# Kernel tuning notes

Hardware: AMD Instinct MI355X
Metric: run time of the kernel (lower is better)

Reference implementation:

```python
import jax, jax.numpy as jnp
import numpy as np

B, L, S, D, H, E, UV = 4, 2048, 2048, 1024, 8, 128, 128
ROT_DIM = H * E  # RotaryEmbedding(dim=qk_size*n_heads) applied on flattened dim


def gelu(x):
    return jax.nn.gelu(x, approximate=False)  # torch nn.GELU default (erf)


def rope(x):
    # x: [B, T, ROT_DIM]; interleaved-pair rotary (lucidrains rotary_embedding_torch default)
    T = x.shape[1]
    inv_freq = 1.0 / (10000.0 ** (jnp.arange(0, ROT_DIM, 2, dtype=jnp.float32) / ROT_DIM))
    freqs = jnp.arange(T, dtype=jnp.float32)[:, None] * inv_freq  # [T, ROT_DIM/2]
    cos = jnp.repeat(jnp.cos(freqs), 2, axis=-1)  # [T, ROT_DIM]
    sin = jnp.repeat(jnp.sin(freqs), 2, axis=-1)
    xp = x.reshape(*x.shape[:-1], ROT_DIM // 2, 2)
    x_rot = jnp.stack([-xp[..., 1], xp[..., 0]], axis=-1).reshape(x.shape)
    return x * cos + x_rot * sin


def setup_inputs() -> dict:
    key = jax.random.key(0)
    ks = jax.random.split(key, 16)
    n = lambda k, sh, s=1.0: jax.random.normal(k, sh, jnp.float32) * s
    w = 0.02
    return {
        "u": n(ks[0], (B, L, D)),
        "queries": n(ks[1], (B, L, D)),
        "keys": n(ks[2], (B, S, D)),
        "values": n(ks[3], (B, S, D)),
        "Wqk": n(ks[4], (D, H * E), w), "bqk": jnp.zeros((H * E,), jnp.float32),
        "Wv": n(ks[5], (D, H * UV), w), "bv": jnp.zeros((H * UV,), jnp.float32),
        "Wu": n(ks[6], (D, H * UV), w), "bu": jnp.zeros((H * UV,), jnp.float32),
        "Wo": n(ks[7], (H * UV, D), w), "bo": jnp.zeros((D,), jnp.float32),
        "q_gamma": jnp.ones((E,), jnp.float32), "q_beta": n(ks[8], (E,), w),
        "k_gamma": jnp.ones((E,), jnp.float32), "k_beta": n(ks[9], (E,), w),
    }


def _forward(u, queries, keys, values, Wqk, bqk, Wv, bv, Wu, bu, Wo, bo,
             q_gamma, q_beta, k_gamma, k_beta):
    # use_aff=True: shared qk projection + per-branch ScaleOffset over qk_size
    qk = gelu(queries @ Wqk + bqk)                      # [B,L,H*E]
    qk4 = qk.reshape(B, L, H, E)
    q = (qk4 * q_gamma + q_beta).reshape(B, L, H * E)
    k = (qk4 * k_gamma + k_beta).reshape(B, L, H * E)
    q = rope(q).reshape(B, L, H, E)
    k = rope(k).reshape(B, S, H, E)
    v = gelu(values @ Wv + bv).reshape(B, S, H, UV)
    # Conv1d(kernel_size=1) == pointwise linear over channels
    u_p = gelu(u @ Wu + bu).reshape(B, L, H, UV)
    scale = 1.0 / jnp.sqrt(jnp.float32(E))
    scores = jnp.einsum("blhe,bshe->bhls", q, k) * scale
    attn = jax.nn.softmax(scores, axis=-1)              # [B,H,L,S]
    ctx = jnp.einsum("bhls,bshd->blhd", attn, v)        # [B,L,H,UV]
    out = (u_p * ctx).reshape(B, L, H * UV)             # gate by u
    o = out @ Wo + bo                                   # [B,L,D]
    return o, attn


def reference(u, queries, keys, values, Wqk, bqk, Wv, bv, Wu, bu, Wo, bo,
              q_gamma, q_beta, k_gamma, k_beta):
    return _forward(u, queries, keys, values, Wqk, bqk, Wv, bv, Wu, bu, Wo, bo,
                    q_gamma, q_beta, k_gamma, k_beta)
```

## Files before the change

kernel.cpp:

```cpp
#include <hip/hip_runtime.h>
#include <hip/hip_bf16.h>
#include <math.h>

#define DEVI static __device__ __forceinline__

typedef __attribute__((ext_vector_type(4))) float f32x4;
typedef __attribute__((ext_vector_type(16))) float f32x16;
typedef __attribute__((ext_vector_type(8))) short bf16x8;
typedef __attribute__((ext_vector_type(4))) short bf16x4;

constexpr int Bc = 4, Lc = 2048, Sc = 2048, Dc = 1024, Hc = 8, Ec = 128, UVc = 128;
constexpr int HEc = Hc * Ec;
constexpr int BLc = Bc * Lc;

#define QSC (1.44269504088896340f / 11.31370849898476039f)

DEVI unsigned f2bf_bits(float f) {
  unsigned u = __builtin_bit_cast(unsigned, f);
  return (u + 0x7FFFu + ((u >> 16) & 1u)) >> 16;
}
DEVI short f2bf(float f) { return (short)f2bf_bits(f); }
DEVI float bf2f(short s) {
  return __builtin_bit_cast(float, (unsigned)((unsigned short)s) << 16);
}
DEVI float gelu_f(float x) {
  float z = fabsf(x) * 0.7071067811865476f;
  float t = __builtin_amdgcn_rcpf(1.0f + 0.3275911f * z);
  float p = t * (0.254829592f +
            t * (-0.284496736f +
            t * (1.421413741f +
            t * (-1.453152027f + t * 1.061405429f))));
  float e = exp2f(-z * z * 1.4426950408889634f);
  float er = copysignf(1.0f - p * e, x);
  return 0.5f * x * (1.0f + er);
}

DEVI void gload16(const void* gsrc, void* ldst) {
  __builtin_amdgcn_global_load_lds(
      (const __attribute__((address_space(1))) unsigned*)gsrc,
      (__attribute__((address_space(3))) unsigned*)(ldst), 16, 0, 0);
}

DEVI f32x4 mfma16(bf16x8 a, bf16x8 b, f32x4 c) {
  return __builtin_amdgcn_mfma_f32_16x16x32_bf16(a, b, c, 0, 0, 0);
}
DEVI f32x16 mfma32(bf16x8 a, bf16x8 b, f32x16 c) {
  return __builtin_amdgcn_mfma_f32_32x32x16_bf16(a, b, c, 0, 0, 0);
}

__global__ void cvt3_kernel(const float* __restrict__ i0, const float* __restrict__ i1,
                            const float* __restrict__ i2, short* __restrict__ o0,
                            short* __restrict__ o1, short* __restrict__ o2) {
  const float* ins[3] = {i0, i1, i2};
  short* outs[3] = {o0, o1, o2};
  const float* in = ins[blockIdx.y];
  short* out = outs[blockIdx.y];
  size_t i = ((size_t)blockIdx.x * 256 + threadIdx.x) * 8;
  float4 f1 = *reinterpret_cast<const float4*>(in + i);
  float4 f2 = *reinterpret_cast<const float4*>(in + i + 4);
  uint4 pk;
  pk.x = f2bf_bits(f1.x) | (f2bf_bits(f1.y) << 16);
  pk.y = f2bf_bits(f1.z) | (f2bf_bits(f1.w) << 16);
  pk.z = f2bf_bits(f2.x) | (f2bf_bits(f2.y) << 16);
  pk.w = f2bf_bits(f2.z) | (f2bf_bits(f2.w) << 16);
  *reinterpret_cast<uint4*>(out + i) = pk;
}

__global__ void prep_kernel(const float* __restrict__ W0, const float* __restrict__ W1,
                            const float* __restrict__ W2, const float* __restrict__ W3,
                            short* __restrict__ T0, short* __restrict__ T1,
                            short* __restrict__ T2, short* __restrict__ T3,
                            float2* __restrict__ cs) {
  int tx = threadIdx.x, ty = threadIdx.y;
  if (blockIdx.z == 4) {
    int base = (blockIdx.y * 32 + blockIdx.x) * 256 + ty * 32 + tx;
#pragma unroll
    for (int j = 0; j < 4; j++) {
      int idx = base + j * 262144;
      int t = idx >> 9, i = idx & 511;
      float inv = expf((float)i * (-9.210340371976184f / 512.0f));
      float sv, cv;
      sincosf((float)t * inv, &sv, &cv);
      cs[idx] = make_float2(cv, sv);
    }
    return;
  }
  __shared__ float tbuf[32][33];
  const float* Ws[4] = {W0, W1, W2, W3};
  short* Ts[4] = {T0, T1, T2, T3};
  const float* W = Ws[blockIdx.z];
  short* WT = Ts[blockIdx.z];
  int n0 = blockIdx.x * 32, k0 = blockIdx.y * 32;
#pragma unroll
  for (int i = 0; i < 4; i++) {
    int r = ty + i * 8;
    tbuf[r][tx] = W[(size_t)(k0 + r) * 1024 + n0 + tx];
  }
  __syncthreads();
#pragma unroll
  for (int i = 0; i < 4; i++) {
    int r = ty + i * 8;
    WT[(size_t)(n0 + r) * 1024 + k0 + tx] = f2bf(tbuf[tx][r]);
  }
}

template <int EPI>
__global__ __launch_bounds__(256, 3) void gemm_kernel(
    const short* __restrict__ A, const short* __restrict__ BT,
    const float* __restrict__ bias, void* __restrict__ Cptr, int M, int N, int K) {
  __shared__ char smem[49152];
  const int tid = threadIdx.x;
  const int wave = tid >> 6, lane = tid & 63;
  const int lquad = lane >> 4, l15 = lane & 15;
  const int m0 = blockIdx.x * 128, n0 = blockIdx.y * 128;
  const int wr = wave >> 1, wc = wave & 1;
  f32x4 acc[4][4] = {};

  const int q0 = tid * 16, q1 = tid * 16 + 4096;
  const int r0 = q0 >> 6, o0 = (q0 & 63) ^ ((r0 & 3) << 4);
  const int r1 = q1 >> 6, o1 = (q1 & 63) ^ ((r1 & 3) << 4);
  const short* a0 = A + (size_t)(m0 + r0) * K + (o0 >> 1);
  const short* a1 = A + (size_t)(m0 + r1) * K + (o1 >> 1);
  const short* b0 = BT + (size_t)(n0 + r0) * K + (o0 >> 1);
  const short* b1 = BT + (size_t)(n0 + r1) * K + (o1 >> 1);

#define G_STAGE(buf, kt)                     \
  {                                          \
    char* As_ = smem + (buf)*8192;           \
    char* Bs_ = smem + 24576 + (buf)*8192;   \
    gload16(a0 + (kt), As_ + q0);            \
    gload16(a1 + (kt), As_ + q1);            \
    gload16(b0 + (kt), Bs_ + q0);            \
    gload16(b1 + (kt), Bs_ + q1);            \
  }

  G_STAGE(0, 0);
  G_STAGE(1, 32);
  asm volatile("s_waitcnt vmcnt(4)" ::: "memory");
  __builtin_amdgcn_s_barrier();

  const int NT = K >> 5;
  int cur = 0;
  for (int t = 0; t < NT; t++) {
    int nb = cur + 2;
    if (nb >= 3) nb -= 3;
    G_STAGE(nb, (t + 2 < NT) ? (t + 2) * 32 : 0);
    __builtin_amdgcn_sched_barrier(0);
    const char* As_ = smem + cur * 8192;
    const char* Bs_ = smem + 24576 + cur * 8192;
    const int ko = lquad * 16;
    bf16x8 a[4], b[4];
#pragma unroll
    for (int f = 0; f < 4; f++) {
      int ra = wr * 64 + f * 16 + l15;
      a[f] = *reinterpret_cast<const bf16x8*>(As_ + ra * 64 + (ko ^ ((ra & 3) << 4)));
      int rb = wc * 64 + f * 16 + l15;
      b[f] = *reinterpret_cast<const bf16x8*>(Bs_ + rb * 64 + (ko ^ ((rb & 3) << 4)));
    }
#pragma unroll
    for (int mf = 0; mf < 4; mf++)
#pragma unroll
      for (int nf = 0; nf < 4; nf++)
        acc[mf][nf] = mfma16(a[mf], b[nf], acc[mf][nf]);
    asm volatile("s_waitcnt vmcnt(4) lgkmcnt(0)" ::: "memory");
    __builtin_amdgcn_sched_barrier(0);
    __builtin_amdgcn_s_barrier();
    cur = (cur == 2) ? 0 : cur + 1;
  }
#undef G_STAGE

#pragma unroll
  for (int mf = 0; mf < 4; mf++) {
#pragma unroll
    for (int nf = 0; nf < 4; nf++) {
      const int mrow = m0 + wr * 64 + mf * 16 + 4 * lquad;
      const int ncol = n0 + wc * 64 + nf * 16 + l15;
      const float bval = bias[ncol];
      if constexpr (EPI == 3) {
        int hh = ncol >> 7, dd = ncol & 127;
        int bb = mrow >> 11, ss = mrow & 2047;
        bf16x4 gv;
#pragma unroll
        for (int r = 0; r < 4; r++) gv[r] = f2bf(gelu_f(acc[mf][nf][r] + bval));
        *reinterpret_cast<bf16x4*>((short*)Cptr + (((size_t)bb * 8 + hh) * 128 + dd) * 2048 + ss) = gv;
      } else if constexpr (EPI == 1) {
#pragma unroll
        for (int r = 0; r < 4; r++)
          ((short*)Cptr)[(size_t)(mrow + r) * N + ncol] = f2bf(gelu_f(acc[mf][nf][r] + bval));
      } else {
#pragma unroll
        for (int r = 0; r < 4; r++)
          ((float*)Cptr)[(size_t)(mrow + r) * N + ncol] = acc[mf][nf][r] + bval;
      }
    }
  }
}

__global__ void rope_apply_kernel(const short* __restrict__ qkg,
                                  const float2* __restrict__ cstab,
                                  const float* __restrict__ qg, const float* __restrict__ qb,
                                  const float* __restrict__ kg, const float* __restrict__ kb,
                                  short* __restrict__ qo, short* __restrict__ ko) {
  int tid = blockIdx.x * 256 + threadIdx.x;
  size_t base = (size_t)tid * 8;
  int bl = (int)(base >> 10);
  int rem = (int)(base & 1023);
  int e0 = rem & 127;
  int t = bl & 2047;
  int pf = rem >> 1;
  uint4 raw = *reinterpret_cast<const uint4*>(qkg + base);
  short sh[8];
  *reinterpret_cast<uint4*>(sh) = raw;
  const float* csf = (const float*)cstab + (size_t)t * 1024 + 2 * pf;
  float4 p01 = *reinterpret_cast<const float4*>(csf);
  float4 p23 = *reinterpret_cast<const float4*>(csf + 4);
  float C[4] = {p01.x, p01.z, p23.x, p23.z};
  float Sn[4] = {p01.y, p01.w, p23.y, p23.w};
  float4 qga = *reinterpret_cast<const float4*>(qg + e0);
  float4 qgb = *reinterpret_cast<const float4*>(qg + e0 + 4);
  float4 qba = *reinterpret_cast<const float4*>(qb + e0);
  float4 qbb = *reinterpret_cast<const float4*>(qb + e0 + 4);
  float4 kga = *reinterpret_cast<const float4*>(kg + e0);
  float4 kgb = *reinterpret_cast<const float4*>(kg + e0 + 4);
  float4 kba = *reinterpret_cast<const float4*>(kb + e0);
  float4 kbb = *reinterpret_cast<const float4*>(kb + e0 + 4);
  float QG[8] = {qga.x, qga.y, qga.z, qga.w, qgb.x, qgb.y, qgb.z, qgb.w};
  float QB[8] = {qba.x, qba.y, qba.z, qba.w, qbb.x, qbb.y, qbb.z, qbb.w};
  float KG[8] = {kga.x, kga.y, kga.z, kga.w, kgb.x, kgb.y, kgb.z, kgb.w};
  float KB[8] = {kba.x, kba.y, kba.z, kba.w, kbb.x, kbb.y, kbb.z, kbb.w};
  short qsh[8], ksh[8];
#pragma unroll
  for (int j = 0; j < 4; j++) {
    float x0 = bf2f(sh[2 * j]), x1 = bf2f(sh[2 * j + 1]);
    float q0 = x0 * QG[2 * j] + QB[2 * j];
    float q1 = x1 * QG[2 * j + 1] + QB[2 * j + 1];
    qsh[2 * j] = f2bf((q0 * C[j] - q1 * Sn[j]) * QSC);
    qsh[2 * j + 1] = f2bf((q1 * C[j] + q0 * Sn[j]) * QSC);
    float k0v = x0 * KG[2 * j] + KB[2 * j];
    float k1v = x1 * KG[2 * j + 1] + KB[2 * j + 1];
    ksh[2 * j] = f2bf(k0v * C[j] - k1v * Sn[j]);
    ksh[2 * j + 1] = f2bf(k1v * C[j] + k0v * Sn[j]);
  }
  *reinterpret_cast<uint4*>(qo + base) = *reinterpret_cast<uint4*>(qsh);
  *reinterpret_cast<uint4*>(ko + base) = *reinterpret_cast<uint4*>(ksh);
}

__global__ __launch_bounds__(256, 3) void passa_kernel(
    const short* __restrict__ qs, const short* __restrict__ ks,
    float* __restrict__ rcpbuf) {
  __shared__ char smem[49152];
  const int bid = blockIdx.x;
  const int xcd = bid & 7, jj = bid >> 3;
  const int bh = xcd * 4 + (jj >> 4);
  const int lblk = jj & 15;
  const int b = bh >> 3, h = bh & 7;
  const int l0 = lblk * 128;
  const int tid = threadIdx.x;
  const int wave = tid >> 6, lane = tid & 63;
  const int l31 = lane & 31, lhg = lane >> 5;

  const short* ksrc[4];
  int kq[4];
#pragma unroll
  for (int i = 0; i < 4; i++) {
    int q = i * 4096 + tid * 16;
    kq[i] = q;
    int row = q >> 8, off = (q & 255) ^ ((row & 7) << 4);
    ksrc[i] = ks + (((size_t)b * Sc + row) * Hc + h) * Ec + (off >> 1);
  }

  bf16x8 qf[8];
  {
    const char* qp = (const char*)(qs + (((size_t)b * Lc + l0 + wave * 32 + l31) * Hc + h) * Ec);
#pragma unroll
    for (int kt = 0; kt < 8; kt++)
      qf[kt] = *reinterpret_cast<const bf16x8*>(qp + kt * 32 + 16 * lhg);
  }
  __builtin_amdgcn_sched_barrier(0);

#define STAGE_A(buf, s0)                                  \
  {                                                       \
    char* Kb_ = smem + (buf)*16384;                       \
    gload16(ksrc[0] + (size_t)(s0)*1024, Kb_ + kq[0]);    \
    gload16(ksrc[1] + (size_t)(s0)*1024, Kb_ + kq[1]);    \
    gload16(ksrc[2] + (size_t)(s0)*1024, Kb_ + kq[2]);    \
    gload16(ksrc[3] + (size_t)(s0)*1024, Kb_ + kq[3]);    \
  }

  STAGE_A(0, 0);
  STAGE_A(1, 64);
  asm volatile("s_waitcnt vmcnt(4)" ::: "memory");
  __builtin_amdgcn_s_barrier();
  float ra = 0.f, rb = 0.f, rc = 0.f, rd = 0.f;
  int cur = 0;
  for (int t = 0; t < 32; t++) {
    int nb = cur + 2;
    if (nb >= 3) nb -= 3;
    STAGE_A(nb, (t + 2 < 32) ? (t + 2) * 64 : 0);
    __builtin_amdgcn_sched_barrier(0);
    const char* KB_ = smem + cur * 16384;
    f32x16 d0 = {}, d1 = {};
    __builtin_amdgcn_s_setprio(1);
#pragma unroll
    for (int kt = 0; kt < 8; kt++) {
      int row0 = l31, row1 = 32 + l31;
      bf16x8 k0 = *reinterpret_cast<const bf16x8*>(
          KB_ + row0 * 256 + ((kt * 32 + 16 * lhg) ^ ((row0 & 7) << 4)));
      bf16x8 k1 = *reinterpret_cast<const bf16x8*>(
          KB_ + row1 * 256 + ((kt * 32 + 16 * lhg) ^ ((row1 & 7) << 4)));
      d0 = mfma32(k0, qf[kt], d0);
      d1 = mfma32(k1, qf[kt], d1);
    }
    __builtin_amdgcn_s_setprio(0);
#pragma unroll
    for (int r = 0; r < 16; r += 4) {
      ra += exp2f(d0[r]) + exp2f(d1[r]);
      rb += exp2f(d0[r + 1]) + exp2f(d1[r + 1]);
      rc += exp2f(d0[r + 2]) + exp2f(d1[r + 2]);
      rd += exp2f(d0[r + 3]) + exp2f(d1[r + 3]);
    }
    asm volatile("s_waitcnt vmcnt(4) lgkmcnt(0)" ::: "memory");
    __builtin_amdgcn_sched_barrier(0);
    __builtin_amdgcn_s_barrier();
    cur = (cur == 2) ? 0 : cur + 1;
  }
#undef STAGE_A
  float rs = (ra + rb) + (rc + rd);
  rs += __shfl_xor(rs, 32);
  if (lane < 32)
    rcpbuf[(size_t)bh * Lc + l0 + wave * 32 + l31] = 1.0f / rs;
}

__global__ __launch_bounds__(256, 3) void attn_kernel(
    const short* __restrict__ qs, const short* __restrict__ ks,
    const short* __restrict__ vT, const short* __restrict__ up,
    const float* __restrict__ rcpbuf, float* __restrict__ attn_out,
    short* __restrict__ gate) {
  __shared__ char smem[49152];
  const int bid = blockIdx.x;
  const int xcd = bid & 7, jj = bid >> 3;
  const int bh = xcd * 4 + (jj >> 4);
  const int lblk = jj & 15;
  const int b = bh >> 3, h = bh & 7;
  const int l0 = lblk * 128;
  const int tid = threadIdx.x;
  const int wave = tid >> 6, lane = tid & 63;
  const int lquad = lane >> 4, l15 = lane & 15;

  const short* ksrc[2];
  int kq[2];
#pragma unroll
  for (int i = 0; i < 2; i++) {
    int q = i * 4096 + tid * 16;
    kq[i] = q;
    int row = q >> 8, off = (q & 255) ^ ((row & 7) << 4);
    ksrc[i] = ks + (((size_t)b * Sc + row) * Hc + h) * Ec + (off >> 1);
  }
  const short* vsrc[2];
  int vq[2];
#pragma unroll
  for (int i = 0; i < 2; i++) {
    int q = i * 4096 + tid * 16;
    vq[i] = q;
    int rv = q >> 6;
    int j = (q >> 4) & 3;
    int c = (j - (rv & 3)) & 3;
    vsrc[i] = vT + ((size_t)bh * UVc + rv) * Sc + (c << 3);
  }

  bf16x8 qf[2][4];
  float rcp[2];
#pragma unroll
  for (int cf = 0; cf < 2; cf++) {
    int lrow = l0 + wave * 32 + cf * 16 + l15;
    const short* qp = qs + (((size_t)b * Lc + lrow) * Hc + h) * Ec;
#pragma unroll
    for (int kt = 0; kt < 4; kt++)
      qf[cf][kt] = *reinterpret_cast<const bf16x8*>(qp + kt * 32 + lquad * 8);
    rcp[cf] = rcpbuf[(size_t)bh * Lc + lrow];
  }
  __builtin_amdgcn_sched_barrier(0);

#define STAGE_B(buf, s0)                                  \
  {                                                       \
    char* Kb_ = smem + (buf)*8192;                        \
    char* Vb_ = smem + 24576 + (buf)*8192;                \
    gload16(ksrc[0] + (size_t)(s0)*1024, Kb_ + kq[0]);    \
    gload16(ksrc[1] + (size_t)(s0)*1024, Kb_ + kq[1]);    \
    gload16(vsrc[0] + (s0), Vb_ + vq[0]);                 \
    gload16(vsrc[1] + (s0), Vb_ + vq[1]);                 \
  }

  STAGE_B(0, 0);
  STAGE_B(1, 32);
  asm volatile("s_waitcnt vmcnt(4)" ::: "memory");
  __builtin_amdgcn_s_barrier();
  f32x4 ctx[8][2] = {};
  int cur = 0;
  for (int t = 0; t < 64; t++) {
    const int s0 = t * 32;
    const char* KB_ = smem + cur * 8192;
    const char* VB_ = smem + 24576 + cur * 8192;
    f32x4 d[2][2] = {};
    __builtin_amdgcn_s_setprio(1);
#pragma unroll
    for (int kt = 0; kt < 4; kt++)
#pragma unroll
      for (int sf = 0; sf < 2; sf++) {
        int row = sf * 16 + l15;
        bf16x8 kf = *reinterpret_cast<const bf16x8*>(
            KB_ + row * 256 + ((kt * 64 + lquad * 16) ^ ((row & 7) << 4)));
        d[sf][0] = mfma16(kf, qf[0][kt], d[sf][0]);
        d[sf][1] = mfma16(kf, qf[1][kt], d[sf][1]);
      }
    __builtin_amdgcn_s_setprio(0);
#pragma unroll
    for (int sf = 0; sf < 2; sf++)
#pragma unroll
      for (int cf = 0; cf < 2; cf++)
#pragma unroll
        for (int r = 0; r < 4; r++)
          d[sf][cf][r] = exp2f(d[sf][cf][r]) * rcp[cf];
#pragma unroll
    for (int cf = 0; cf < 2; cf++) {
      int lrow = l0 + wave * 32 + cf * 16 + l15;
      float* arow = attn_out + ((size_t)bh * Lc + lrow) * Sc + s0 + lquad * 4;
      __builtin_nontemporal_store(d[0][cf], reinterpret_cast<f32x4*>(arow));
      __builtin_nontemporal_store(d[1][cf], reinterpret_cast<f32x4*>(arow + 16));
    }
    bf16x8 pb[2];
#pragma unroll
    for (int cf = 0; cf < 2; cf++)
#pragma unroll
      for (int r = 0; r < 4; r++) {
        pb[cf][r] = f2bf(d[0][cf][r]);
        pb[cf][4 + r] = f2bf(d[1][cf][r]);
      }
    __builtin_amdgcn_s_setprio(1);
#pragma unroll
    for (int df = 0; df < 8; df++) {
      int dd = df * 16 + l15;
      const char* vrow = VB_ + dd * 64;
      int half = (lquad & 1) * 8;
      int clo = ((lquad >> 1) + (dd & 3)) & 3;
      int chi = ((lquad >> 1) + 2 + (dd & 3)) & 3;
      bf16x4 lo = *reinterpret_cast<const bf16x4*>(vrow + clo * 16 + half);
      bf16x4 hi = *reinterpret_cast<const bf16x4*>(vrow + chi * 16 + half);
      bf16x8 vf = __builtin_shufflevector(lo, hi, 0, 1, 2, 3, 4, 5, 6, 7);
      ctx[df][0] = mfma16(vf, pb[0], ctx[df][0]);
      ctx[df][1] = mfma16(vf, pb[1], ctx[df][1]);
    }
    __builtin_amdgcn_s_setprio(0);
    {
      int nb = cur + 2;
      if (nb >= 3) nb -= 3;
      STAGE_B(nb, (t + 2 < 64) ? s0 + 64 : 0);
    }
    asm volatile("s_waitcnt vmcnt(8) lgkmcnt(0)" ::: "memory");
    __builtin_amdgcn_sched_barrier(0);
    __builtin_amdgcn_s_barrier();
    cur = (cur == 2) ? 0 : cur + 1;
  }
#undef STAGE_B

#pragma unroll
  for (int cf = 0; cf < 2; cf++) {
    int lrow = l0 + wave * 32 + cf * 16 + l15;
    size_t base = ((size_t)b * Lc + lrow) * HEc + h * UVc;
    const short* ub = up + base;
    short* gp = gate + base;
#pragma unroll
    for (int df = 0; df < 8; df++) {
      int doff = df * 16 + lquad * 4;
      bf16x4 uv = *reinterpret_cast<const bf16x4*>(ub + doff);
      bf16x4 gv;
#pragma unroll
      for (int r = 0; r < 4; r++)
        gv[r] = f2bf(bf2f(uv[r]) * ctx[df][cf][r]);
      *reinterpret_cast<bf16x4*>(gp + doff) = gv;
    }
  }
}

extern "C" void kernel_launch(void* const* d_in, const int* in_sizes, int n_in,
                              void* d_out, int out_size, void* d_ws, size_t ws_size,
                              hipStream_t stream) {
  const float* u_in = (const float*)d_in[0];
  const float* qry = (const float*)d_in[1];
  const float* vals = (const float*)d_in[3];
  const float* Wqk = (const float*)d_in[4];
  const float* bqk = (const float*)d_in[5];
  const float* Wv = (const float*)d_in[6];
  const float* bv = (const float*)d_in[7];
  const float* Wu = (const float*)d_in[8];
  const float* bu = (const float*)d_in[9];
  const float* Wo = (const float*)d_in[10];
  const float* bo = (const float*)d_in[11];
  const float* qg = (const float*)d_in[12];
  const float* qb = (const float*)d_in[13];
  const float* kg = (const float*)d_in[14];
  const float* kb = (const float*)d_in[15];

  char* w = (char*)d_ws;
  short* WT0 = (short*)w; w += (size_t)1024 * 1024 * 2;
  short* WT1 = (short*)w; w += (size_t)1024 * 1024 * 2;
  short* WT2 = (short*)w; w += (size_t)1024 * 1024 * 2;
  short* WT3 = (short*)w; w += (size_t)1024 * 1024 * 2;
  float2* cstab = (float2*)w; w += (size_t)2048 * 512 * 8;
  float* rcpb = (float*)w; w += (size_t)32 * 2048 * 4;
  const size_t BUF = (size_t)BLc * HEc * 2;
  short* C1 = (short*)w; w += BUF;
  short* C2 = (short*)w; w += BUF;
  short* C3 = (short*)w; w += BUF;
  short* qkg = (short*)w; w += BUF;
  short* qbf = (short*)w; w += BUF;
  short* vTb = (short*)w; w += BUF;
  short* upb = (short*)w; w += BUF;
  short* kbf = qkg;
  short* gtb = C1;

  float* o_out = (float*)d_out;
  float* attn_out = o_out + (size_t)BLc * Dc;

  dim3 tb(32, 8);
  cvt3_kernel<<<dim3(4096, 3), 256, 0, stream>>>(qry, vals, u_in, C1, C2, C3);
  prep_kernel<<<dim3(32, 32, 5), tb, 0, stream>>>(Wqk, Wv, Wu, Wo, WT0, WT1, WT2, WT3, cstab);

  gemm_kernel<1><<<dim3(64, 8), 256, 0, stream>>>(C1, WT0, bqk, qkg, BLc, HEc, Dc);
  rope_apply_kernel<<<4096, 256, 0, stream>>>(qkg, cstab, qg, qb, kg, kb, qbf, kbf);
  passa_kernel<<<512, 256, 0, stream>>>(qbf, kbf, rcpb);
  gemm_kernel<3><<<dim3(64, 8), 256, 0, stream>>>(C2, WT1, bv, vTb, BLc, HEc, Dc);
  gemm_kernel<1><<<dim3(64, 8), 256, 0, stream>>>(C3, WT2, bu, upb, BLc, HEc, Dc);
  attn_kernel<<<512, 256, 0, stream>>>(qbf, kbf, vTb, upb, rcpb, attn_out, gtb);
  gemm_kernel<0><<<dim3(64, 8), 256, 0, stream>>>(gtb, WT3, bo, o_out, BLc, Dc, HEc);
}
```

Baseline: 387.2 us.

## Fuse RoPE and scale-offset into QK GEMM epilogue; merge prep kernels

The QK projection GEMM now applies GELU, the per-branch scale/offset and rotary embedding in its epilogue. It gets each rotary partner value via a lane xor-shuffle and writes q and k bf16 directly, so the separate rope kernel and its intermediate buffer round trip go away. The input conversion, weight transpose and cos/sin table kernels are merged into one launch to cut launch overhead. In exchange, the epilogue stores become scattered 2-byte writes and the kernel reads the cos/sin table from global memory per element.

After: 378.8 us. 1.02x faster.

```diff
diff --git a/kernel.cpp b/kernel.cpp
--- a/kernel.cpp
+++ b/kernel.cpp
@@ -48,81 +48,106 @@
   return __builtin_amdgcn_mfma_f32_32x32x16_bf16(a, b, c, 0, 0, 0);
 }
 
-__global__ void cvt3_kernel(const float* __restrict__ i0, const float* __restrict__ i1,
-                            const float* __restrict__ i2, short* __restrict__ o0,
-                            short* __restrict__ o1, short* __restrict__ o2) {
-  const float* ins[3] = {i0, i1, i2};
-  short* outs[3] = {o0, o1, o2};
-  const float* in = ins[blockIdx.y];
-  short* out = outs[blockIdx.y];
-  size_t i = ((size_t)blockIdx.x * 256 + threadIdx.x) * 8;
-  float4 f1 = *reinterpret_cast<const float4*>(in + i);
-  float4 f2 = *reinterpret_cast<const float4*>(in + i + 4);
-  uint4 pk;
-  pk.x = f2bf_bits(f1.x) | (f2bf_bits(f1.y) << 16);
-  pk.y = f2bf_bits(f1.z) | (f2bf_bits(f1.w) << 16);
-  pk.z = f2bf_bits(f2.x) | (f2bf_bits(f2.y) << 16);
-  pk.w = f2bf_bits(f2.z) | (f2bf_bits(f2.w) << 16);
-  *reinterpret_cast<uint4*>(out + i) = pk;
-}
-
-__global__ void prep_kernel(const float* __restrict__ W0, const float* __restrict__ W1,
-                            const float* __restrict__ W2, const float* __restrict__ W3,
-                            short* __restrict__ T0, short* __restrict__ T1,
-                            short* __restrict__ T2, short* __restrict__ T3,
-                            float2* __restrict__ cs) {
-  int tx = threadIdx.x, ty = threadIdx.y;
-  if (blockIdx.z == 4) {
-    int base = (blockIdx.y * 32 + blockIdx.x) * 256 + ty * 32 + tx;
+__global__ void prep_all_kernel(const float* __restrict__ in_q, const float* __restrict__ in_v,
+                                const float* __restrict__ in_u, short* __restrict__ C1,
+                                short* __restrict__ C2, short* __restrict__ C3,
+                                const float* __restrict__ W0, const float* __restrict__ W1,
+                                const float* __restrict__ W2, const float* __restrict__ W3,
+                                short* __restrict__ T0, short* __restrict__ T1,
+                                short* __restrict__ T2, short* __restrict__ T3,
+                                float2* __restrict__ cs) {
+  __shared__ float tbuf[32][33];
+  const int bid = blockIdx.x;
+  const int t = threadIdx.x;
+  if (bid < 12288) {
+    int which = bid >> 12, blk = bid & 4095;
+    const float* in = (which == 0) ? in_q : (which == 1) ? in_v : in_u;
+    short* out = (which == 0) ? C1 : (which == 1) ? C2 : C3;
+    size_t i = ((size_t)blk * 256 + t) * 8;
+    float4 f1 = *reinterpret_cast<const float4*>(in + i);
+    float4 f2 = *reinterpret_cast<const float4*>(in + i + 4);
+    uint4 pk;
+    pk.x = f2bf_bits(f1.x) | (f2bf_bits(f1.y) << 16);
+    pk.y = f2bf_bits(f1.z) | (f2bf_bits(f1.w) << 16);
+    pk.z = f2bf_bits(f2.x) | (f2bf_bits(f2.y) << 16);
+    pk.w = f2bf_bits(f2.z) | (f2bf_bits(f2.w) << 16);
+    *reinterpret_cast<uint4*>(out + i) = pk;
+  } else if (bid < 17408) {
+    int z = (bid - 12288) >> 10, rem = (bid - 12288) & 1023;
+    int n0 = (rem & 31) * 32, k0 = (rem >> 5) * 32;
+    int tx = t & 31, ty = t >> 5;
+    const float* Ws[4] = {W0, W1, W2, W3};
+    short* Ts[4] = {T0, T1, T2, T3};
+    const float* W = Ws[z];
+    short* WT = Ts[z];
+#pragma unroll
+    for (int i = 0; i < 4; i++) {
+      int r = ty + i * 8;
+      tbuf[r][tx] = W[(size_t)(k0 + r) * 1024 + n0 + tx];
+    }
+    __syncthreads();
+#pragma unroll
+    for (int i = 0; i < 4; i++) {
+      int r = ty + i * 8;
+      WT[(size_t)(n0 + r) * 1024 + k0 + tx] = f2bf(tbuf[tx][r]);
+    }
+  } else {
+    int base = (bid - 17408) * 256 + t;
 #pragma unroll
     for (int j = 0; j < 4; j++) {
       int idx = base + j * 262144;
-      int t = idx >> 9, i = idx & 511;
+      int tt = idx >> 9, i = idx & 511;
       float inv = expf((float)i * (-9.210340371976184f / 512.0f));
       float sv, cv;
-      sincosf((float)t * inv, &sv, &cv);
+      sincosf((float)tt * inv, &sv, &cv);
       cs[idx] = make_float2(cv, sv);
     }
-    return;
-  }
-  __shared__ float tbuf[32][33];
-  const float* Ws[4] = {W0, W1, W2, W3};
-  short* Ts[4] = {T0, T1, T2, T3};
-  const float* W = Ws[blockIdx.z];
-  short* WT = Ts[blockIdx.z];
-  int n0 = blockIdx.x * 32, k0 = blockIdx.y * 32;
-#pragma unroll
-  for (int i = 0; i < 4; i++) {
-    int r = ty + i * 8;
-    tbuf[r][tx] = W[(size_t)(k0 + r) * 1024 + n0 + tx];
-  }
-  __syncthreads();
-#pragma unroll
-  for (int i = 0; i < 4; i++) {
-    int r = ty + i * 8;
-    WT[(size_t)(n0 + r) * 1024 + k0 + tx] = f2bf(tbuf[tx][r]);
-  }
-}
-
-template <int EPI>
-__global__ __launch_bounds__(256, 3) void gemm_kernel(
-    const short* __restrict__ A, const short* __restrict__ BT,
-    const float* __restrict__ bias, void* __restrict__ Cptr, int M, int N, int K) {
-  __shared__ char smem[49152];
-  const int tid = threadIdx.x;
-  const int wave = tid >> 6, lane = tid & 63;
-  const int lquad = lane >> 4, l15 = lane & 15;
-  const int m0 = blockIdx.x * 128, n0 = blockIdx.y * 128;
-  const int wr = wave >> 1, wc = wave & 1;
-  f32x4 acc[4][4] = {};
-
-  const int q0 = tid * 16, q1 = tid * 16 + 4096;
-  const int r0 = q0 >> 6, o0 = (q0 & 63) ^ ((r0 & 3) << 4);
-  const int r1 = q1 >> 6, o1 = (q1 & 63) ^ ((r1 & 3) << 4);
-  const short* a0 = A + (size_t)(m0 + r0) * K + (o0 >> 1);
-  const short* a1 = A + (size_t)(m0 + r1) * K + (o1 >> 1);
-  const short* b0 = BT + (size_t)(n0 + r0) * K + (o0 >> 1);
-  const short* b1 = BT + (size_t)(n0 + r1) * K + (o1 >> 1);
+  }
+}
+
+#define GEMM_MAIN_LOOP(A, BT, K)                                                     \
+  const int tid = threadIdx.x;                                                       \
+  const int wave = tid >> 6, lane = tid & 63;                                        \
+  const int lquad = lane >> 4, l15 = lane & 15;                                      \
+  const int m0 = blockIdx.x * 128, n0 = blockIdx.y * 128;                            \
+  const int wr = wave >> 1, wc = wave & 1;                                           \
+  f32x4 acc[4][4] = {};                                                              \
+  const int q0 = tid * 16, q1 = tid * 16 + 4096;                                     \
+  const int r0 = q0 >> 6, o0 = (q0 & 63) ^ ((r0 & 3) << 4);                          \
+  const int r1 = q1 >> 6, o1 = (q1 & 63) ^ ((r1 & 3) << 4);                          \
+  const short* a0 = (A) + (size_t)(m0 + r0) * (K) + (o0 >> 1);                       \
+  const short* a1 = (A) + (size_t)(m0 + r1) * (K) + (o1 >> 1);                       \
+  const short* b0 = (BT) + (size_t)(n0 + r0) * (K) + (o0 >> 1);                      \
+  const short* b1 = (BT) + (size_t)(n0 + r1) * (K) + (o1 >> 1);                      \
+  G_STAGE(0, 0);                                                                     \
+  G_STAGE(1, 32);                                                                    \
+  asm volatile("s_waitcnt vmcnt(4)" ::: "memory");                                   \
+  __builtin_amdgcn_s_barrier();                                                      \
+  const int NT = (K) >> 5;                                                           \
+  int cur = 0;                                                                       \
+  for (int t = 0; t < NT; t++) {                                                     \
+    int nb = cur + 2;                                                                \
+    if (nb >= 3) nb -= 3;                                                            \
+    G_STAGE(nb, (t + 2 < NT) ? (t + 2) * 32 : 0);                                    \
+    __builtin_amdgcn_sched_barrier(0);                                               \
+    const char* As_ = smem + cur * 8192;                                             \
+    const char* Bs_ = smem + 24576 + cur * 8192;                                     \
+    const int ko = lquad * 16;                                                       \
+    bf16x8 a[4], b[4];                                                               \
+    _Pragma("unroll") for (int f = 0; f < 4; f++) {                                  \
+      int ra = wr * 64 + f * 16 + l15;                                               \
+      a[f] = *reinterpret_cast<const bf16x8*>(As_ + ra * 64 + (ko ^ ((ra & 3) << 4)));\
+      int rb = wc * 64 + f * 16 + l15;                                               \
+      b[f] = *reinterpret_cast<const bf16x8*>(Bs_ + rb * 64 + (ko ^ ((rb & 3) << 4)));\
+    }                                                                                \
+    _Pragma("unroll") for (int mf = 0; mf < 4; mf++)                                 \
+      _Pragma("unroll") for (int nf = 0; nf < 4; nf++)                               \
+        acc[mf][nf] = mfma16(a[mf], b[nf], acc[mf][nf]);                             \
+    asm volatile("s_waitcnt vmcnt(4) lgkmcnt(0)" ::: "memory");                      \
+    __builtin_amdgcn_sched_barrier(0);                                               \
+    __builtin_amdgcn_s_barrier();                                                    \
+    cur = (cur == 2) ? 0 : cur + 1;                                                  \
+  }
 
 #define G_STAGE(buf, kt)                     \
   {                                          \
@@ -134,41 +159,12 @@
     gload16(b1 + (kt), Bs_ + q1);            \
   }
 
-  G_STAGE(0, 0);
-  G_STAGE(1, 32);
-  asm volatile("s_waitcnt vmcnt(4)" ::: "memory");
-  __builtin_amdgcn_s_barrier();
-
-  const int NT = K >> 5;
-  int cur = 0;
-  for (int t = 0; t < NT; t++) {
-    int nb = cur + 2;
-    if (nb >= 3) nb -= 3;
-    G_STAGE(nb, (t + 2 < NT) ? (t + 2) * 32 : 0);
-    __builtin_amdgcn_sched_barrier(0);
-    const char* As_ = smem + cur * 8192;
-    const char* Bs_ = smem + 24576 + cur * 8192;
-    const int ko = lquad * 16;
-    bf16x8 a[4], b[4];
-#pragma unroll
-    for (int f = 0; f < 4; f++) {
-      int ra = wr * 64 + f * 16 + l15;
-      a[f] = *reinterpret_cast<const bf16x8*>(As_ + ra * 64 + (ko ^ ((ra & 3) << 4)));
-      int rb = wc * 64 + f * 16 + l15;
-      b[f] = *reinterpret_cast<const bf16x8*>(Bs_ + rb * 64 + (ko ^ ((rb & 3) << 4)));
-    }
-#pragma unroll
-    for (int mf = 0; mf < 4; mf++)
-#pragma unroll
-      for (int nf = 0; nf < 4; nf++)
-        acc[mf][nf] = mfma16(a[mf], b[nf], acc[mf][nf]);
-    asm volatile("s_waitcnt vmcnt(4) lgkmcnt(0)" ::: "memory");
-    __builtin_amdgcn_sched_barrier(0);
-    __builtin_amdgcn_s_barrier();
-    cur = (cur == 2) ? 0 : cur + 1;
-  }
-#undef G_STAGE
-
+template <int EPI>
+__global__ __launch_bounds__(256, 3) void gemm_kernel(
+    const short* __restrict__ A, const short* __restrict__ BT,
+    const float* __restrict__ bias, void* __restrict__ Cptr, int M, int N, int K) {
+  __shared__ char smem[49152];
+  GEMM_MAIN_LOOP(A, BT, K)
 #pragma unroll
   for (int mf = 0; mf < 4; mf++) {
 #pragma unroll
@@ -196,54 +192,41 @@
   }
 }
 
-__global__ void rope_apply_kernel(const short* __restrict__ qkg,
-                                  const float2* __restrict__ cstab,
-                                  const float* __restrict__ qg, const float* __restrict__ qb,
-                                  const float* __restrict__ kg, const float* __restrict__ kb,
-                                  short* __restrict__ qo, short* __restrict__ ko) {
-  int tid = blockIdx.x * 256 + threadIdx.x;
-  size_t base = (size_t)tid * 8;
-  int bl = (int)(base >> 10);
-  int rem = (int)(base & 1023);
-  int e0 = rem & 127;
-  int t = bl & 2047;
-  int pf = rem >> 1;
-  uint4 raw = *reinterpret_cast<const uint4*>(qkg + base);
-  short sh[8];
-  *reinterpret_cast<uint4*>(sh) = raw;
-  const float* csf = (const float*)cstab + (size_t)t * 1024 + 2 * pf;
-  float4 p01 = *reinterpret_cast<const float4*>(csf);
-  float4 p23 = *reinterpret_cast<const float4*>(csf + 4);
-  float C[4] = {p01.x, p01.z, p23.x, p23.z};
-  float Sn[4] = {p01.y, p01.w, p23.y, p23.w};
-  float4 qga = *reinterpret_cast<const float4*>(qg + e0);
-  float4 qgb = *reinterpret_cast<const float4*>(qg + e0 + 4);
-  float4 qba = *reinterpret_cast<const float4*>(qb + e0);
-  float4 qbb = *reinterpret_cast<const float4*>(qb + e0 + 4);
-  float4 kga = *reinterpret_cast<const float4*>(kg + e0);
-  float4 kgb = *reinterpret_cast<const float4*>(kg + e0 + 4);
-  float4 kba = *reinterpret_cast<const float4*>(kb + e0);
-  float4 kbb = *reinterpret_cast<const float4*>(kb + e0 + 4);
-  float QG[8] = {qga.x, qga.y, qga.z, qga.w, qgb.x, qgb.y, qgb.z, qgb.w};
-  float QB[8] = {qba.x, qba.y, qba.z, qba.w, qbb.x, qbb.y, qbb.z, qbb.w};
-  float KG[8] = {kga.x, kga.y, kga.z, kga.w, kgb.x, kgb.y, kgb.z, kgb.w};
-  float KB[8] = {kba.x, kba.y, kba.z, kba.w, kbb.x, kbb.y, kbb.z, kbb.w};
-  short qsh[8], ksh[8];
-#pragma unroll
-  for (int j = 0; j < 4; j++) {
-    float x0 = bf2f(sh[2 * j]), x1 = bf2f(sh[2 * j + 1]);
-    float q0 = x0 * QG[2 * j] + QB[2 * j];
-    float q1 = x1 * QG[2 * j + 1] + QB[2 * j + 1];
-    qsh[2 * j] = f2bf((q0 * C[j] - q1 * Sn[j]) * QSC);
-    qsh[2 * j + 1] = f2bf((q1 * C[j] + q0 * Sn[j]) * QSC);
-    float k0v = x0 * KG[2 * j] + KB[2 * j];
-    float k1v = x1 * KG[2 * j + 1] + KB[2 * j + 1];
-    ksh[2 * j] = f2bf(k0v * C[j] - k1v * Sn[j]);
-    ksh[2 * j + 1] = f2bf(k1v * C[j] + k0v * Sn[j]);
-  }
-  *reinterpret_cast<uint4*>(qo + base) = *reinterpret_cast<uint4*>(qsh);
-  *reinterpret_cast<uint4*>(ko + base) = *reinterpret_cast<uint4*>(ksh);
-}
+__global__ __launch_bounds__(256, 3) void gemm_rope_kernel(
+    const short* __restrict__ A, const short* __restrict__ BT,
+    const float* __restrict__ bias, const float2* __restrict__ cstab,
+    const float* __restrict__ qg, const float* __restrict__ qb,
+    const float* __restrict__ kg, const float* __restrict__ kb,
+    short* __restrict__ qout, short* __restrict__ kout) {
+  __shared__ char smem[49152];
+  GEMM_MAIN_LOOP(A, BT, Dc)
+#pragma unroll
+  for (int mf = 0; mf < 4; mf++) {
+#pragma unroll
+    for (int nf = 0; nf < 4; nf++) {
+      const int mrow = m0 + wr * 64 + mf * 16 + 4 * lquad;
+      const int ncol = n0 + wc * 64 + nf * 16 + l15;
+      const float bval = bias[ncol];
+      const int e7 = ncol & 127;
+      const float QG = qg[e7], QB = qb[e7], KG = kg[e7], KB = kb[e7];
+      const int p = ncol >> 1;
+      const float sgn = (ncol & 1) ? 1.0f : -1.0f;
+#pragma unroll
+      for (int r = 0; r < 4; r++) {
+        const int m = mrow + r;
+        const int tt = m & 2047;
+        float2 cs = cstab[(size_t)tt * 512 + p];
+        float g = gelu_f(acc[mf][nf][r] + bval);
+        float qv = g * QG + QB, kv = g * KG + KB;
+        float pq = __shfl_xor(qv, 1), pk = __shfl_xor(kv, 1);
+        qout[(size_t)m * HEc + ncol] = f2bf((qv * cs.x + sgn * pq * cs.y) * QSC);
+        kout[(size_t)m * HEc + ncol] = f2bf(kv * cs.x + sgn * pk * cs.y);
+      }
+    }
+  }
+}
+#undef G_STAGE
+#undef GEMM_MAIN_LOOP
 
 __global__ __launch_bounds__(256, 3) void passa_kernel(
     const short* __restrict__ qs, const short* __restrict__ ks,
@@ -512,22 +495,19 @@
   short* C1 = (short*)w; w += BUF;
   short* C2 = (short*)w; w += BUF;
   short* C3 = (short*)w; w += BUF;
-  short* qkg = (short*)w; w += BUF;
   short* qbf = (short*)w; w += BUF;
+  short* kbf = (short*)w; w += BUF;
   short* vTb = (short*)w; w += BUF;
   short* upb = (short*)w; w += BUF;
-  short* kbf = qkg;
   short* gtb = C1;
 
   float* o_out = (float*)d_out;
   float* attn_out = o_out + (size_t)BLc * Dc;
 
-  dim3 tb(32, 8);
-  cvt3_kernel<<<dim3(4096, 3), 256, 0, stream>>>(qry, vals, u_in, C1, C2, C3);
-  prep_kernel<<<dim3(32, 32, 5), tb, 0, stream>>>(Wqk, Wv, Wu, Wo, WT0, WT1, WT2, WT3, cstab);
-
-  gemm_kernel<1><<<dim3(64, 8), 256, 0, stream>>>(C1, WT0, bqk, qkg, BLc, HEc, Dc);
-  rope_apply_kernel<<<4096, 256, 0, stream>>>(qkg, cstab, qg, qb, kg, kb, qbf, kbf);
+  prep_all_kernel<<<18432, 256, 0, stream>>>(qry, vals, u_in, C1, C2, C3, Wqk, Wv, Wu, Wo,
+                                             WT0, WT1, WT2, WT3, cstab);
+  gemm_rope_kernel<<<dim3(64, 8), 256, 0, stream>>>(C1, WT0, bqk, cstab, qg, qb, kg, kb,
+                                                    qbf, kbf);
   passa_kernel<<<512, 256, 0, stream>>>(qbf, kbf, rcpb);
   gemm_kernel<3><<<dim3(64, 8), 256, 0, stream>>>(C2, WT1, bv, vTb, BLc, HEc, Dc);
   gemm_kernel<1><<<dim3(64, 8), 256, 0, stream>>>(C3, WT2, bu, upb, BLc, HEc, Dc);
```
